# Kernel optimization log

Measured on AMD Instinct MI355X. Metric: run time of the kernel, lower is better.

The kernel has to match this reference:

```python
import jax, jax.numpy as jnp
import numpy as np

D = 1024
H = 16


def setup_inputs() -> dict:
    key = jax.random.key(0)
    ks = jax.random.split(key, 5)
    s = 1.0 / np.sqrt(D)
    x = jax.random.normal(ks[0], (4, 1024, D), dtype=jnp.float32)
    W_qkv = jax.random.normal(ks[1], (D, 3 * D), dtype=jnp.float32) * s
    b_qkv = jnp.zeros((3 * D,), dtype=jnp.float32)
    W_out = jax.random.normal(ks[2], (D, D), dtype=jnp.float32) * s
    b_out = jnp.zeros((D,), dtype=jnp.float32)
    return {"x": x, "W_qkv": W_qkv, "b_qkv": b_qkv, "W_out": W_out, "b_out": b_out}


def reference(x, W_qkv, b_qkv, W_out, b_out):
    bs, ns, d = x.shape
    dh = d // H
    scale = 1.0 / np.sqrt(dh)
    qkv = x @ W_qkv + b_qkv                      # [B,S,3D]
    qkv = qkv.reshape(bs, ns, 3, H, dh)
    q, k, v = qkv[:, :, 0], qkv[:, :, 1], qkv[:, :, 2]  # [B,S,H,dh]
    # attention scores [B,H,S,S]
    attn = jnp.einsum('bqhd,bkhd->bhqk', q, k) * scale
    attn = jax.nn.softmax(attn, axis=-1)
    out = jnp.einsum('bhqk,bkhd->bqhd', attn, v)  # [B,S,H,dh]
    out = out.reshape(bs, ns, d)
    return out @ W_out + b_out
```

## Files before the change

kernel.cpp:

```cpp
#include <hip/hip_runtime.h>
#include <hip/hip_bf16.h>
#include <cstdint>

typedef __bf16 bf16x8 __attribute__((ext_vector_type(8)));
typedef float f32x4 __attribute__((ext_vector_type(4)));

__device__ __forceinline__ unsigned short f2b(float f) {
  __bf16 h = (__bf16)f;
  return __builtin_bit_cast(unsigned short, h);
}

__device__ __forceinline__ void gload_lds16(const void* g, void* l) {
  __builtin_amdgcn_global_load_lds(
      (__attribute__((address_space(1))) void*)g,
      (__attribute__((address_space(3))) void*)l,
      16, 0, 0);
}

__global__ void cvt_f32_bf16(const float* __restrict__ in,
                             unsigned short* __restrict__ out, int n) {
  int i = (blockIdx.x * blockDim.x + threadIdx.x) * 4;
  if (i + 3 < n) {
    float4 f = *(const float4*)&in[i];
    ushort4 u = make_ushort4(f2b(f.x), f2b(f.y), f2b(f.z), f2b(f.w));
    *(ushort4*)&out[i] = u;
  }
}

__global__ void transpose_cvt(const float* __restrict__ in,
                              unsigned short* __restrict__ out, int R, int C) {
  __shared__ float tile[32][33];
  int c0 = blockIdx.x * 32, r0 = blockIdx.y * 32;
  int x = threadIdx.x, y = threadIdx.y;
  #pragma unroll
  for (int j = y; j < 32; j += 8)
    tile[j][x] = in[(size_t)(r0 + j) * C + c0 + x];
  __syncthreads();
  #pragma unroll
  for (int j = y; j < 32; j += 8)
    out[(size_t)(c0 + j) * R + r0 + x] = f2b(tile[x][j]);
}

__global__ void transpose_v(const unsigned short* __restrict__ qkv,
                            unsigned short* __restrict__ vt) {
  __shared__ unsigned short tile[32][33];
  int bh = blockIdx.x, s0 = blockIdx.y * 32, d0 = blockIdx.z * 32;
  int b = bh >> 4, h = bh & 15;
  int x = threadIdx.x, y = threadIdx.y;
  #pragma unroll
  for (int j = y; j < 32; j += 8)
    tile[j][x] = qkv[(size_t)(b * 1024 + s0 + j) * 3072 + 2048 + h * 64 + d0 + x];
  __syncthreads();
  #pragma unroll
  for (int j = y; j < 32; j += 8)
    vt[(size_t)(bh * 64 + d0 + j) * 1024 + s0 + x] = tile[x][j];
}

template <int OUT_F32>
__global__ __launch_bounds__(256, 2)
void gemm_bt(const unsigned short* __restrict__ A,
             const unsigned short* __restrict__ Bt,
             const float* __restrict__ bias, void* __restrict__ C,
             int M, int N, int K) {
  __shared__ __align__(16) unsigned short sA[128 * 32];
  __shared__ __align__(16) unsigned short sB[128 * 32];
  const int t = threadIdx.x;
  const int w = t >> 6, lane = t & 63;
  const int ln = lane & 15, lq = lane >> 4;
  const int wr = w >> 1, wc = w & 1;
  const int m0 = blockIdx.y * 128, n0 = blockIdx.x * 128;

  f32x4 acc[4][4];
  #pragma unroll
  for (int i = 0; i < 4; i++)
    #pragma unroll
    for (int j = 0; j < 4; j++) acc[i][j] = (f32x4){0.f, 0.f, 0.f, 0.f};

  for (int k0 = 0; k0 < K; k0 += 32) {
    __syncthreads();
    #pragma unroll
    for (int i = 0; i < 2; ++i) {
      int idx = i * 256 + t;
      int row = idx >> 2;
      int cb = (idx & 3) * 8;
      gload_lds16(A + (size_t)(m0 + row) * K + k0 + cb, &sA[idx * 8]);
    }
    #pragma unroll
    for (int i = 0; i < 2; ++i) {
      int idx = i * 256 + t;
      int row = idx >> 2;
      int cb = (idx & 3) * 8;
      gload_lds16(Bt + (size_t)(n0 + row) * K + k0 + cb, &sB[idx * 8]);
    }
    __syncthreads();
    bf16x8 af[4], bfr[4];
    #pragma unroll
    for (int m = 0; m < 4; m++)
      af[m] = *(const bf16x8*)&sA[(wr * 64 + m * 16 + ln) * 32 + lq * 8];
    #pragma unroll
    for (int n = 0; n < 4; n++)
      bfr[n] = *(const bf16x8*)&sB[(wc * 64 + n * 16 + ln) * 32 + lq * 8];
    #pragma unroll
    for (int m = 0; m < 4; m++)
      #pragma unroll
      for (int n = 0; n < 4; n++)
        acc[m][n] = __builtin_amdgcn_mfma_f32_16x16x32_bf16(af[m], bfr[n], acc[m][n], 0, 0, 0);
  }

  #pragma unroll
  for (int m = 0; m < 4; m++) {
    #pragma unroll
    for (int n = 0; n < 4; n++) {
      int col = n0 + wc * 64 + n * 16 + ln;
      float bv = bias[col];
      #pragma unroll
      for (int r = 0; r < 4; r++) {
        int row = m0 + wr * 64 + m * 16 + lq * 4 + r;
        float v = acc[m][n][r] + bv;
        if (OUT_F32)
          ((float*)C)[(size_t)row * N + col] = v;
        else
          ((unsigned short*)C)[(size_t)row * N + col] = f2b(v);
      }
    }
  }
}

__global__ __launch_bounds__(256, 4)
void attn_fwd(const unsigned short* __restrict__ qkv,
              const unsigned short* __restrict__ vt,
              unsigned short* __restrict__ aout) {
  const int b = blockIdx.z, h = blockIdx.y, q0 = blockIdx.x * 64;
  __shared__ __align__(16) unsigned short sB[4][64 * 64];
  __shared__ __align__(16) unsigned short sP[4][16 * 64];
  const int t = threadIdx.x;
  const int w = t >> 6, lane = t & 63;
  const int ln = lane & 15, lq = lane >> 4;
  const float SCALE = 0.125f;

  const size_t qbase = (size_t)(b * 1024 + q0) * 3072 + h * 64;
  const size_t kbase = (size_t)(b * 1024) * 3072 + 1024 + h * 64;
  const size_t vbase = (size_t)((b * 16 + h) * 64) * 1024;

  #pragma unroll
  for (int i = 0; i < 2; i++) {
    int idx = i * 256 + t;
    int row = idx >> 3, ch = idx & 7;
    int sw = (ch ^ (row & 7)) * 8;
    gload_lds16(qkv + qbase + (size_t)row * 3072 + sw, &sB[0][idx * 8]);
    gload_lds16(qkv + kbase + (size_t)row * 3072 + sw, &sB[1][idx * 8]);
    gload_lds16(vt + vbase + (size_t)row * 1024 + sw, &sB[2][idx * 8]);
  }
  __syncthreads();
  bf16x8 qf[2];
  #pragma unroll
  for (int c = 0; c < 2; c++) {
    int row = w * 16 + ln;
    qf[c] = *(const bf16x8*)&sB[0][row * 64 + ((c * 4 + lq) ^ (ln & 7)) * 8];
  }
  __syncthreads();

  f32x4 o[4];
  float mrow = -1e30f, lsum = 0.f;
  #pragma unroll
  for (int n = 0; n < 4; n++) o[n] = (f32x4){0.f, 0.f, 0.f, 0.f};

  for (int kt = 0; kt < 16; ++kt) {
    const unsigned short* kb = sB[(kt & 1) ? 3 : 1];
    const unsigned short* vb = sB[(kt & 1) ? 0 : 2];
    if (kt < 15) {
      const int kv1 = (kt + 1) * 64;
      unsigned short* kn = sB[(kt & 1) ? 1 : 3];
      unsigned short* vn = sB[(kt & 1) ? 2 : 0];
      #pragma unroll
      for (int i = 0; i < 2; i++) {
        int idx = i * 256 + t;
        int row = idx >> 3, ch = idx & 7;
        int sw = (ch ^ (row & 7)) * 8;
        gload_lds16(qkv + kbase + (size_t)(kv1 + row) * 3072 + sw, &kn[idx * 8]);
        gload_lds16(vt + vbase + (size_t)row * 1024 + kv1 + sw, &vn[idx * 8]);
      }
    }

    f32x4 st[4];
    #pragma unroll
    for (int kc = 0; kc < 4; kc++) st[kc] = (f32x4){0.f, 0.f, 0.f, 0.f};
    #pragma unroll
    for (int kc = 0; kc < 4; kc++) {
      int krow = kc * 16 + ln;
      bf16x8 k0f = *(const bf16x8*)&kb[krow * 64 + ((0 + lq) ^ (ln & 7)) * 8];
      bf16x8 k1f = *(const bf16x8*)&kb[krow * 64 + ((4 + lq) ^ (ln & 7)) * 8];
      st[kc] = __builtin_amdgcn_mfma_f32_16x16x32_bf16(k0f, qf[0], st[kc], 0, 0, 0);
      st[kc] = __builtin_amdgcn_mfma_f32_16x16x32_bf16(k1f, qf[1], st[kc], 0, 0, 0);
    }

    float xv[4][4];
    float tm = -1e30f;
    #pragma unroll
    for (int kc = 0; kc < 4; kc++) {
      #pragma unroll
      for (int r = 0; r < 4; r++) {
        xv[kc][r] = st[kc][r] * SCALE;
        tm = fmaxf(tm, xv[kc][r]);
      }
    }
    tm = fmaxf(tm, __shfl_xor(tm, 16));
    tm = fmaxf(tm, __shfl_xor(tm, 32));
    float mn = fmaxf(mrow, tm);
    float al = __expf(mrow - mn);
    mrow = mn;
    float ts = 0.f;
    #pragma unroll
    for (int kc = 0; kc < 4; kc++) {
      #pragma unroll
      for (int r = 0; r < 4; r++) {
        xv[kc][r] = __expf(xv[kc][r] - mn);
        ts += xv[kc][r];
      }
    }
    ts += __shfl_xor(ts, 16);
    ts += __shfl_xor(ts, 32);
    lsum = lsum * al + ts;

    #pragma unroll
    for (int r = 0; r < 4; r++) {
      float alr = __shfl(al, (lane & 48) | (lq * 4 + r));
      #pragma unroll
      for (int n = 0; n < 4; n++) o[n][r] *= alr;
    }

    unsigned char* pb = (unsigned char*)sP[w];
    #pragma unroll
    for (int kc = 0; kc < 4; kc++) {
      ushort4 u = make_ushort4(f2b(xv[kc][0]), f2b(xv[kc][1]),
                               f2b(xv[kc][2]), f2b(xv[kc][3]));
      int boff = (kc * 32 + lq * 8) ^ ((ln & 7) << 4);
      *(ushort4*)(pb + ln * 128 + boff) = u;
    }

    #pragma unroll
    for (int c2 = 0; c2 < 2; c2++) {
      bf16x8 pa = *(const bf16x8*)&sP[w][ln * 64 + ((c2 * 4 + lq) ^ (ln & 7)) * 8];
      #pragma unroll
      for (int n = 0; n < 4; n++) {
        int vrow = n * 16 + ln;
        bf16x8 vf = *(const bf16x8*)&vb[vrow * 64 + ((c2 * 4 + lq) ^ (ln & 7)) * 8];
        o[n] = __builtin_amdgcn_mfma_f32_16x16x32_bf16(pa, vf, o[n], 0, 0, 0);
      }
    }

    asm volatile("s_waitcnt vmcnt(0)" ::: "memory");
    __builtin_amdgcn_s_barrier();
  }

  float linv[4];
  #pragma unroll
  for (int r = 0; r < 4; r++)
    linv[r] = 1.f / __shfl(lsum, (lane & 48) | (lq * 4 + r));
  #pragma unroll
  for (int n = 0; n < 4; n++) {
    #pragma unroll
    for (int r = 0; r < 4; r++) {
      int row = q0 + w * 16 + lq * 4 + r;
      int col = h * 64 + n * 16 + ln;
      aout[(size_t)(b * 1024 + row) * 1024 + col] = f2b(o[n][r] * linv[r]);
    }
  }
}

extern "C" void kernel_launch(void* const* d_in, const int* in_sizes, int n_in,
                              void* d_out, int out_size, void* d_ws, size_t ws_size,
                              hipStream_t stream) {
  const float* x = (const float*)d_in[0];
  const float* W_qkv = (const float*)d_in[1];
  const float* b_qkv = (const float*)d_in[2];
  const float* W_out = (const float*)d_in[3];
  const float* b_out = (const float*)d_in[4];
  float* out = (float*)d_out;

  char* ws = (char*)d_ws;
  unsigned short* xb    = (unsigned short*)(ws);
  unsigned short* wqkvT = (unsigned short*)(ws + 8388608);
  unsigned short* woutT = (unsigned short*)(ws + 14680064);
  unsigned short* qkv   = (unsigned short*)(ws + 16777216);
  unsigned short* vt    = (unsigned short*)(ws + 41943040);
  unsigned short* aout  = (unsigned short*)(ws + 50331648);
  if (ws_size < 58720256) return;

  cvt_f32_bf16<<<4096, 256, 0, stream>>>(x, xb, 4096 * 1024);
  transpose_cvt<<<dim3(96, 32), dim3(32, 8), 0, stream>>>(W_qkv, wqkvT, 1024, 3072);
  transpose_cvt<<<dim3(32, 32), dim3(32, 8), 0, stream>>>(W_out, woutT, 1024, 1024);
  gemm_bt<0><<<dim3(24, 32), 256, 0, stream>>>(xb, wqkvT, b_qkv, qkv, 4096, 3072, 1024);
  transpose_v<<<dim3(64, 32, 2), dim3(32, 8), 0, stream>>>(qkv, vt);
  attn_fwd<<<dim3(16, 16, 4), 256, 0, stream>>>(qkv, vt, aout);
  gemm_bt<1><<<dim3(8, 32), 256, 0, stream>>>(aout, woutT, b_out, out, 4096, 1024, 1024);
}
```

Measured before the change: 125.2 us.

## Double-buffer GEMM LDS tiles, add MFMA priority hints, lazy softmax rescale with exp2

The GEMM kernel now double-buffers its A/B LDS tiles, issuing the next k-slice load before computing the current one, with one barrier per iteration. Both kernels wrap MFMA blocks in s_setprio to favour matrix issue. Attention switches to exp2 with the log2e factor folded into the scale, and skips the running-max rescale of the output and sum unless the max grows by more than a threshold. The aim is to hide global-load latency and cut per-tile softmax work. The cost is doubled GEMM LDS, which may lower occupancy, and the lazy rescale tolerates larger exponent ranges before updating.

```diff
diff --git a/kernel.cpp b/kernel.cpp
--- a/kernel.cpp
+++ b/kernel.cpp
@@ -62,8 +62,8 @@
              const unsigned short* __restrict__ Bt,
              const float* __restrict__ bias, void* __restrict__ C,
              int M, int N, int K) {
-  __shared__ __align__(16) unsigned short sA[128 * 32];
-  __shared__ __align__(16) unsigned short sB[128 * 32];
+  __shared__ __align__(16) unsigned short sA[2][128 * 32];
+  __shared__ __align__(16) unsigned short sB[2][128 * 32];
   const int t = threadIdx.x;
   const int w = t >> 6, lane = t & 63;
   const int ln = lane & 15, lq = lane >> 4;
@@ -76,35 +76,49 @@
     #pragma unroll
     for (int j = 0; j < 4; j++) acc[i][j] = (f32x4){0.f, 0.f, 0.f, 0.f};
 
-  for (int k0 = 0; k0 < K; k0 += 32) {
-    __syncthreads();
+  auto stage = [&](int buf, int k0) {
     #pragma unroll
     for (int i = 0; i < 2; ++i) {
       int idx = i * 256 + t;
       int row = idx >> 2;
       int cb = (idx & 3) * 8;
-      gload_lds16(A + (size_t)(m0 + row) * K + k0 + cb, &sA[idx * 8]);
+      gload_lds16(A + (size_t)(m0 + row) * K + k0 + cb, &sA[buf][idx * 8]);
     }
     #pragma unroll
     for (int i = 0; i < 2; ++i) {
       int idx = i * 256 + t;
       int row = idx >> 2;
       int cb = (idx & 3) * 8;
-      gload_lds16(Bt + (size_t)(n0 + row) * K + k0 + cb, &sB[idx * 8]);
-    }
-    __syncthreads();
+      gload_lds16(Bt + (size_t)(n0 + row) * K + k0 + cb, &sB[buf][idx * 8]);
+    }
+  };
+
+  stage(0, 0);
+  asm volatile("s_waitcnt vmcnt(0)" ::: "memory");
+  __builtin_amdgcn_s_barrier();
+
+  const int nk = K >> 5;
+  for (int ki = 0; ki < nk; ++ki) {
+    const int cur = ki & 1;
+    if (ki + 1 < nk) stage(cur ^ 1, (ki + 1) << 5);
+
     bf16x8 af[4], bfr[4];
     #pragma unroll
     for (int m = 0; m < 4; m++)
-      af[m] = *(const bf16x8*)&sA[(wr * 64 + m * 16 + ln) * 32 + lq * 8];
+      af[m] = *(const bf16x8*)&sA[cur][(wr * 64 + m * 16 + ln) * 32 + lq * 8];
     #pragma unroll
     for (int n = 0; n < 4; n++)
-      bfr[n] = *(const bf16x8*)&sB[(wc * 64 + n * 16 + ln) * 32 + lq * 8];
+      bfr[n] = *(const bf16x8*)&sB[cur][(wc * 64 + n * 16 + ln) * 32 + lq * 8];
+    __builtin_amdgcn_s_setprio(1);
     #pragma unroll
     for (int m = 0; m < 4; m++)
       #pragma unroll
       for (int n = 0; n < 4; n++)
         acc[m][n] = __builtin_amdgcn_mfma_f32_16x16x32_bf16(af[m], bfr[n], acc[m][n], 0, 0, 0);
+    __builtin_amdgcn_s_setprio(0);
+
+    asm volatile("s_waitcnt vmcnt(0)" ::: "memory");
+    __builtin_amdgcn_s_barrier();
   }
 
   #pragma unroll
@@ -136,7 +150,8 @@
   const int t = threadIdx.x;
   const int w = t >> 6, lane = t & 63;
   const int ln = lane & 15, lq = lane >> 4;
-  const float SCALE = 0.125f;
+  const float K2 = 0.125f * 1.44269504f;
+  const float THR = 11.54f;
 
   const size_t qbase = (size_t)(b * 1024 + q0) * 3072 + h * 64;
   const size_t kbase = (size_t)(b * 1024) * 3072 + 1024 + h * 64;
@@ -184,14 +199,14 @@
 
     f32x4 st[4];
     #pragma unroll
-    for (int kc = 0; kc < 4; kc++) st[kc] = (f32x4){0.f, 0.f, 0.f, 0.f};
-    #pragma unroll
     for (int kc = 0; kc < 4; kc++) {
       int krow = kc * 16 + ln;
       bf16x8 k0f = *(const bf16x8*)&kb[krow * 64 + ((0 + lq) ^ (ln & 7)) * 8];
       bf16x8 k1f = *(const bf16x8*)&kb[krow * 64 + ((4 + lq) ^ (ln & 7)) * 8];
-      st[kc] = __builtin_amdgcn_mfma_f32_16x16x32_bf16(k0f, qf[0], st[kc], 0, 0, 0);
+      __builtin_amdgcn_s_setprio(1);
+      st[kc] = __builtin_amdgcn_mfma_f32_16x16x32_bf16(k0f, qf[0], (f32x4){0.f, 0.f, 0.f, 0.f}, 0, 0, 0);
       st[kc] = __builtin_amdgcn_mfma_f32_16x16x32_bf16(k1f, qf[1], st[kc], 0, 0, 0);
+      __builtin_amdgcn_s_setprio(0);
     }
 
     float xv[4][4];
@@ -200,34 +215,38 @@
     for (int kc = 0; kc < 4; kc++) {
       #pragma unroll
       for (int r = 0; r < 4; r++) {
-        xv[kc][r] = st[kc][r] * SCALE;
+        xv[kc][r] = st[kc][r] * K2;
         tm = fmaxf(tm, xv[kc][r]);
       }
     }
     tm = fmaxf(tm, __shfl_xor(tm, 16));
     tm = fmaxf(tm, __shfl_xor(tm, 32));
-    float mn = fmaxf(mrow, tm);
-    float al = __expf(mrow - mn);
-    mrow = mn;
+
+    if (!__all(tm <= mrow + THR)) {
+      float mn = fmaxf(mrow, tm);
+      float al = exp2f(mrow - mn);
+      mrow = mn;
+      lsum *= al;
+      #pragma unroll
+      for (int r = 0; r < 4; r++) {
+        float alr = __shfl(al, (lane & 48) | (lq * 4 + r));
+        #pragma unroll
+        for (int n = 0; n < 4; n++) o[n][r] *= alr;
+      }
+    }
+
     float ts = 0.f;
     #pragma unroll
     for (int kc = 0; kc < 4; kc++) {
       #pragma unroll
       for (int r = 0; r < 4; r++) {
-        xv[kc][r] = __expf(xv[kc][r] - mn);
+        xv[kc][r] = exp2f(xv[kc][r] - mrow);
         ts += xv[kc][r];
       }
     }
     ts += __shfl_xor(ts, 16);
     ts += __shfl_xor(ts, 32);
-    lsum = lsum * al + ts;
-
-    #pragma unroll
-    for (int r = 0; r < 4; r++) {
-      float alr = __shfl(al, (lane & 48) | (lq * 4 + r));
-      #pragma unroll
-      for (int n = 0; n < 4; n++) o[n][r] *= alr;
-    }
+    lsum += ts;
 
     unsigned char* pb = (unsigned char*)sP[w];
     #pragma unroll
@@ -241,12 +260,14 @@
     #pragma unroll
     for (int c2 = 0; c2 < 2; c2++) {
       bf16x8 pa = *(const bf16x8*)&sP[w][ln * 64 + ((c2 * 4 + lq) ^ (ln & 7)) * 8];
+      __builtin_amdgcn_s_setprio(1);
       #pragma unroll
       for (int n = 0; n < 4; n++) {
         int vrow = n * 16 + ln;
         bf16x8 vf = *(const bf16x8*)&vb[vrow * 64 + ((c2 * 4 + lq) ^ (ln & 7)) * 8];
         o[n] = __builtin_amdgcn_mfma_f32_16x16x32_bf16(pa, vf, o[n], 0, 0, 0);
       }
+      __builtin_amdgcn_s_setprio(0);
     }
 
     asm volatile("s_waitcnt vmcnt(0)" ::: "memory");
```

Result: no change. 126.1 us (+0.7%).
